# Optimization experiments

Hardware: AMD Instinct MI355X
Metric: run time of the kernel (lower is better)

Reference implementation:

```python
import jax, jax.numpy as jnp
import numpy as np

NUM_QUANTIZERS = 8
CODEBOOK_SIZE = 4096
DIM = 128
BATCH = 8
SEQ = 4096


def setup_inputs() -> dict:
    key = jax.random.key(0)
    k1, k2 = jax.random.split(key)
    x = jax.random.normal(k1, (BATCH, DIM, SEQ), dtype=jnp.float32)
    codebooks = jax.random.normal(k2, (NUM_QUANTIZERS, CODEBOOK_SIZE, DIM), dtype=jnp.float32)
    return {"x": x, "codebooks": codebooks}


def _rvq(x_bnc, codebooks):
    """Residual VQ: sequential per-stage nearest-codebook quantization.

    x_bnc: [b, n, d]; codebooks: [Q, K, d].
    Returns quantized [b, n, d], indices [b, n, Q], loss scalar.
    """
    residual = x_bnc
    quantized_out = jnp.zeros_like(x_bnc)
    all_indices = []
    all_losses = []
    Q = codebooks.shape[0]
    for q in range(Q):
        cb = codebooks[q]                                   # [K, d]
        # squared-euclidean distances: ||r||^2 - 2 r.c + ||c||^2  -> [b, n, K]
        r_sq = jnp.sum(residual * residual, axis=-1, keepdims=True)
        c_sq = jnp.sum(cb * cb, axis=-1)
        dots = jnp.einsum('bnd,kd->bnk', residual, cb)
        dist = r_sq - 2.0 * dots + c_sq
        idx = jnp.argmin(dist, axis=-1)                      # [b, n]
        quant = cb[idx]                                      # [b, n, d] gather
        # straight-through estimator (grad flows to residual, not codebook)
        quant_st = residual + jax.lax.stop_gradient(quant - residual)
        quantized_out = quantized_out + quant_st
        # commitment loss (codebook is EMA-updated, so detach the quantized side)
        all_losses.append(jnp.mean((jax.lax.stop_gradient(quant) - residual) ** 2))
        residual = residual - jax.lax.stop_gradient(quant)
        all_indices.append(idx)
    indices = jnp.stack(all_indices, axis=-1)                # [b, n, Q]
    loss = jnp.mean(jnp.stack(all_losses))
    return quantized_out, indices, loss


def reference(x, codebooks):
    # encode(): 'b c n -> b n c', quantize, 'b n c -> b c n'
    x_bnc = jnp.transpose(x, (0, 2, 1))
    quant, indices, loss = _rvq(x_bnc, codebooks)
    out = jnp.transpose(quant, (0, 2, 1))                    # [b, c, n]
    return out, indices, loss
```

## Files before the change

### kernel.cpp

```cpp
#include <hip/hip_runtime.h>

typedef _Float16 half8 __attribute__((ext_vector_type(8)));
typedef float    float4v __attribute__((ext_vector_type(4)));
typedef unsigned int u32;

#define NQ 8
#define KCODES 4096
#define DIMS 128
#define BATCH 8
#define SEQ 4096
#define ROWS (BATCH*SEQ)
#define TM 64
#define NBLK (ROWS/TM)
#define RESPAD 132
#define CANDROW 67
#define OUT_ELEMS (BATCH*DIMS*SEQ)
#define IDX_ELEMS (BATCH*SEQ*NQ)
#define LOSS_DIV (1.0f/33554432.0f)
#define FRAGQ ((size_t)4*256*64*8)
#define SBIAS 384.0f
#define WIN 2.0f

__device__ __forceinline__ unsigned umax_(unsigned a, unsigned b){ return a>b?a:b; }
__device__ __forceinline__ unsigned umin_(unsigned a, unsigned b){ return a<b?a:b; }

__device__ __forceinline__ void gload16(const void* g, void* l) {
    __builtin_amdgcn_global_load_lds(
        (const __attribute__((address_space(1))) u32*)g,
        (__attribute__((address_space(3))) u32*)l, 16, 0, 0);
}

__global__ void prep_csq(const float* __restrict__ cb, float* __restrict__ csq,
                         _Float16* __restrict__ cinit_h) {
    int c = blockIdx.x * 256 + threadIdx.x;
    const float4* p = (const float4*)(cb + (size_t)c * DIMS);
    float s = 0.f;
#pragma unroll
    for (int i = 0; i < 32; ++i) {
        float4 v = p[i];
        s += v.x * v.x + v.y * v.y + v.z * v.z + v.w * v.w;
    }
    csq[c] = s;
    cinit_h[c] = (_Float16)(SBIAS - 0.5f * s);
}

__global__ void prep_frags(const float* __restrict__ cb, _Float16* __restrict__ bhi,
                           float* __restrict__ loss_accum) {
    int g = blockIdx.x * 256 + threadIdx.x;
    if (g == 0) loss_accum[0] = 0.f;
    int lane = g & 63;
    int nt   = (g >> 6) & 255;
    int kb   = (g >> 14) & 3;
    int q    = g >> 16;
    int code = nt * 16 + (lane & 15);
    int k0   = kb * 32 + ((lane >> 4) * 8);
    const float* src = cb + ((size_t)q * KCODES + code) * DIMS + k0;
    float4 v0 = *(const float4*)(src);
    float4 v1 = *(const float4*)(src + 4);
    half8 h;
    h[0] = (_Float16)v0.x; h[1] = (_Float16)v0.y; h[2] = (_Float16)v0.z; h[3] = (_Float16)v0.w;
    h[4] = (_Float16)v1.x; h[5] = (_Float16)v1.y; h[6] = (_Float16)v1.z; h[7] = (_Float16)v1.w;
    *(half8*)(bhi + (size_t)g * 8) = h;
}

__device__ __forceinline__ void screen_tile(
        int t, int ntBase, int lane, int col,
        char* stgw, const _Float16* __restrict__ bq, const _Float16* cql,
        const half8 (&ahi)[4][4], unsigned (&p1)[4][4], unsigned (&p2)[4][4]) {
    int nt = ntBase + t;
    const half8* sp = (const half8*)(stgw + ((t & 1) << 12) + (lane << 4));
    half8 b0 = sp[0], b1 = sp[64], b2 = sp[128], b3 = sp[192];
    float csv = (float)cql[nt * 16 + col];

    asm volatile("s_waitcnt lgkmcnt(0)" ::: "memory");

    {
        int ntn = ntBase + ((t + 2) & 63);
        char* dst = stgw + ((t & 1) << 12);
#pragma unroll
        for (int kb = 0; kb < 4; ++kb) {
            const _Float16* g = bq + (((size_t)(kb * 256 + ntn) * 64 + lane) << 3);
            gload16(g, dst + (kb << 10));
        }
    }
    asm volatile("s_waitcnt vmcnt(4)" ::: "memory");

    float4v acc[4];
#pragma unroll
    for (int mt = 0; mt < 4; ++mt) { acc[mt][0]=0.f; acc[mt][1]=0.f; acc[mt][2]=0.f; acc[mt][3]=0.f; }
    __builtin_amdgcn_s_setprio(1);
#pragma unroll
    for (int mt = 0; mt < 4; ++mt) acc[mt] = __builtin_amdgcn_mfma_f32_16x16x32_f16(ahi[mt][0], b0, acc[mt], 0, 0, 0);
#pragma unroll
    for (int mt = 0; mt < 4; ++mt) acc[mt] = __builtin_amdgcn_mfma_f32_16x16x32_f16(ahi[mt][1], b1, acc[mt], 0, 0, 0);
#pragma unroll
    for (int mt = 0; mt < 4; ++mt) acc[mt] = __builtin_amdgcn_mfma_f32_16x16x32_f16(ahi[mt][2], b2, acc[mt], 0, 0, 0);
#pragma unroll
    for (int mt = 0; mt < 4; ++mt) acc[mt] = __builtin_amdgcn_mfma_f32_16x16x32_f16(ahi[mt][3], b3, acc[mt], 0, 0, 0);
    __builtin_amdgcn_s_setprio(0);

    unsigned idxv = (unsigned)(nt * 16 + col);
#pragma unroll
    for (int mt = 0; mt < 4; ++mt)
#pragma unroll
        for (int r = 0; r < 4; ++r) {
            float key = acc[mt][r] + csv;
            unsigned p  = (__float_as_uint(key) & 0xFFFFF000u) | idxv;
            unsigned t1 = umin_(p1[mt][r], p);
            p1[mt][r]   = umax_(p1[mt][r], p);
            p2[mt][r]   = umax_(p2[mt][r], t1);
        }
}

__launch_bounds__(256, 2)
__global__ void rvq_main(const float* __restrict__ x, const float* __restrict__ cb,
                         const _Float16* __restrict__ bhi,
                         const float* __restrict__ csq, const _Float16* __restrict__ cinit_h,
                         float* __restrict__ out, float* __restrict__ loss_accum) {
    __shared__ float res[TM][RESPAD];
    __shared__ __align__(16) char stg[4][8192];
    __shared__ __align__(16) _Float16 cinq_lds[KCODES];
    __shared__ float fbin[TM];
    unsigned (*cand)[CANDROW] = reinterpret_cast<unsigned (*)[CANDROW]>(&stg[0][0]);
    float* red = reinterpret_cast<float*>(&stg[0][0] + 20480);

    int tid  = threadIdx.x;
    int lane = tid & 63;
    int wv   = tid >> 6;
    int col  = lane & 15;
    int r0   = blockIdx.x * TM;
    int b    = r0 >> 12;
    int n0   = r0 & (SEQ - 1);
    const float* xb = x + (size_t)b * DIMS * SEQ + n0;

    {
        int d = tid >> 1, half = (tid & 1) * 32;
        const float* src = xb + (size_t)d * SEQ + half;
#pragma unroll
        for (int t4 = 0; t4 < 8; ++t4) {
            float4 v = *(const float4*)(src + t4 * 4);
            res[half + t4 * 4 + 0][d] = v.x;
            res[half + t4 * 4 + 1][d] = v.y;
            res[half + t4 * 4 + 2][d] = v.z;
            res[half + t4 * 4 + 3][d] = v.w;
        }
    }

    float lossacc = 0.f;
    int ntBase = wv * 64;
    char* stgw = &stg[wv][0];

    for (int q = 0; q < NQ; ++q) {
        __syncthreads();

        const _Float16* bq   = bhi + (size_t)q * FRAGQ;
        const _Float16* cq   = cinit_h + q * KCODES;
        const float*    csqq = csq + q * KCODES;

        {
            const _Float16* g0 = cq + wv * 1024 + lane * 8;
            gload16(g0,       (char*)cinq_lds + wv * 2048);
            gload16(g0 + 512, (char*)cinq_lds + wv * 2048 + 1024);
        }
#pragma unroll
        for (int tt = 0; tt < 2; ++tt) {
            char* dst = stgw + (tt << 12);
            int g = ntBase + tt;
#pragma unroll
            for (int kb = 0; kb < 4; ++kb)
                gload16(bq + (((size_t)(kb * 256 + g) * 64 + lane) << 3), dst + (kb << 10));
        }

        half8 ahi[4][4];
#pragma unroll
        for (int mt = 0; mt < 4; ++mt)
#pragma unroll
        for (int kb = 0; kb < 4; ++kb) {
            int row = mt * 16 + col;
            int k0  = kb * 32 + (lane >> 4) * 8;
            float4 v0 = *(const float4*)&res[row][k0];
            float4 v1 = *(const float4*)&res[row][k0 + 4];
            half8 h;
            h[0] = (_Float16)v0.x; h[1] = (_Float16)v0.y; h[2] = (_Float16)v0.z; h[3] = (_Float16)v0.w;
            h[4] = (_Float16)v1.x; h[5] = (_Float16)v1.y; h[6] = (_Float16)v1.z; h[7] = (_Float16)v1.w;
            ahi[mt][kb] = h;
        }

        unsigned p1[4][4], p2[4][4];
#pragma unroll
        for (int mt = 0; mt < 4; ++mt)
#pragma unroll
        for (int r = 0; r < 4; ++r) { p1[mt][r] = 0u; p2[mt][r] = 0u; }

        asm volatile("s_waitcnt vmcnt(4)" ::: "memory");

        for (int t = 0; t < 64; t += 2) {
            screen_tile(t,     ntBase, lane, col, stgw, bq, cinq_lds, ahi, p1, p2);
            screen_tile(t + 1, ntBase, lane, col, stgw, bq, cinq_lds, ahi, p1, p2);
        }
        asm volatile("s_waitcnt vmcnt(0)" ::: "memory");
        __syncthreads();

#pragma unroll
        for (int mt = 0; mt < 4; ++mt)
#pragma unroll
        for (int r = 0; r < 4; ++r) {
            unsigned a1 = p1[mt][r], a2 = p2[mt][r];
            unsigned b1 = (unsigned)__shfl_xor((int)a1, 1, 64);
            unsigned b2 = (unsigned)__shfl_xor((int)a2, 1, 64);
            unsigned n1 = umax_(a1, b1);
            unsigned n2 = umax_(umin_(a1, b1), umax_(a2, b2));
            if ((lane & 1) == 0) {
                int row = mt * 16 + (lane >> 4) * 4 + r;
                int cc  = wv * 16 + (col >> 1) * 2;
                cand[row][cc]     = n1;
                cand[row][cc + 1] = n2;
            }
        }
        __syncthreads();

        {
            int row = tid >> 2, s = tid & 3;
            const unsigned* cp = &cand[row][s * 16];
            unsigned m = 0;
#pragma unroll
            for (int k = 0; k < 16; ++k) m = umax_(m, cp[k]);
            m = umax_(m, (unsigned)__shfl_xor((int)m, 1, 64));
            m = umax_(m, (unsigned)__shfl_xor((int)m, 2, 64));
            float thr = __uint_as_float(m) - WIN;
            float bk = -3.4e38f;
            int   bi = KCODES;
            const float4* rv = (const float4*)&res[row][0];
            for (int k = 0; k < 16; ++k) {
                unsigned e = cp[k];
                if (__uint_as_float(e) >= thr) {
                    int idx = (int)(e & 0xFFFu);
                    const float4* cv = (const float4*)(cb + ((size_t)q * KCODES + idx) * DIMS);
                    float acc = 0.f;
#pragma unroll
                    for (int jj = 0; jj < 32; ++jj) {
                        float4 c4 = cv[jj];
                        float4 r4 = rv[jj];
                        acc = fmaf(r4.x, c4.x, acc);
                        acc = fmaf(r4.y, c4.y, acc);
                        acc = fmaf(r4.z, c4.z, acc);
                        acc = fmaf(r4.w, c4.w, acc);
                    }
                    float key = acc - 0.5f * csqq[idx];
                    if (key > bk || (key == bk && idx < bi)) { bk = key; bi = idx; }
                }
            }
#pragma unroll
            for (int mask = 1; mask <= 2; mask <<= 1) {
                float ok = __shfl_xor(bk, mask, 64);
                int   oi = __shfl_xor(bi, mask, 64);
                if (ok > bk || (ok == bk && oi < bi)) { bk = ok; bi = oi; }
            }
            if (s == 0) {
                fbin[row] = (float)bi;
                out[OUT_ELEMS + (size_t)(r0 + row) * NQ + q] = (float)bi;
            }
        }
        __syncthreads();

        {
            int row = tid >> 2, j = tid & 3;
            int bi = (int)fbin[row];
            const float* cv = cb + ((size_t)q * KCODES + bi) * DIMS + j * 32;
            float* rp = &res[row][j * 32];
#pragma unroll
            for (int t = 0; t < 8; ++t) {
                float4 c4 = *(const float4*)(cv + t * 4);
                float4 r4 = *(const float4*)(rp + t * 4);
                r4.x -= c4.x; lossacc = fmaf(r4.x, r4.x, lossacc);
                r4.y -= c4.y; lossacc = fmaf(r4.y, r4.y, lossacc);
                r4.z -= c4.z; lossacc = fmaf(r4.z, r4.z, lossacc);
                r4.w -= c4.w; lossacc = fmaf(r4.w, r4.w, lossacc);
                *(float4*)(rp + t * 4) = r4;
            }
        }
    }

    __syncthreads();
    red[tid] = lossacc;
    __syncthreads();
    for (int s = 128; s > 0; s >>= 1) {
        if (tid < s) red[tid] += red[tid + s];
        __syncthreads();
    }
    if (tid == 0) atomicAdd(loss_accum, red[0]);

    {
        int d = tid >> 1, half = (tid & 1) * 32;
        const float* src = xb + (size_t)d * SEQ + half;
        float* dst = out + (size_t)b * DIMS * SEQ + (size_t)d * SEQ + n0 + half;
#pragma unroll
        for (int t4 = 0; t4 < 8; ++t4) {
            float4 v = *(const float4*)(src + t4 * 4);
            v.x -= res[half + t4 * 4 + 0][d];
            v.y -= res[half + t4 * 4 + 1][d];
            v.z -= res[half + t4 * 4 + 2][d];
            v.w -= res[half + t4 * 4 + 3][d];
            *(float4*)(dst + t4 * 4) = v;
        }
    }
}

__global__ void finish_loss(const float* __restrict__ loss_accum, float* __restrict__ out) {
    out[OUT_ELEMS + IDX_ELEMS] = loss_accum[0] * LOSS_DIV;
}

extern "C" void kernel_launch(void* const* d_in, const int* in_sizes, int n_in,
                              void* d_out, int out_size, void* d_ws, size_t ws_size,
                              hipStream_t stream) {
    const float* x  = (const float*)d_in[0];
    const float* cb = (const float*)d_in[1];
    float* out = (float*)d_out;
    char*  ws  = (char*)d_ws;

    float*     loss_accum = (float*)ws;
    float*     csq     = (float*)(ws + 256);
    _Float16*  cinit_h = (_Float16*)(ws + 256 + 131072);
    _Float16*  bhi     = (_Float16*)(ws + 256 + 131072 + 65536);

    hipLaunchKernelGGL(prep_csq,   dim3(128),  dim3(256), 0, stream, cb, csq, cinit_h);
    hipLaunchKernelGGL(prep_frags, dim3(2048), dim3(256), 0, stream, cb, bhi, loss_accum);
    hipLaunchKernelGGL(rvq_main,   dim3(NBLK), dim3(256), 0, stream,
                       x, cb, bhi, csq, cinit_h, out, loss_accum);
    hipLaunchKernelGGL(finish_loss, dim3(1), dim3(1), 0, stream, loss_accum, out);
}
```

Baseline: 575.5 us.

## Stream codebook fragments straight to registers with a four-deep inline-asm pipeline

The codebook MFMA B-fragments are no longer staged through LDS with global_load_lds. They are now loaded directly into VGPRs with inline-asm global_load_dwordx4, and a rotating four-tile register pipeline is gated by s_waitcnt vmcnt(8). The per-code bias is folded into the accumulator initial value, which removes an add per output, and the LDS staging buffer is replaced with dedicated cand/red arrays. This removes LDS write and read traffic and the lgkmcnt waits from the inner screening loop. In exchange it raises VGPR pressure and issues prefetch loads past the last tile. Those loads may still be outstanding when the loop exits, and the compiler does not track them.

Result: faster. 527.9 us (-8.3%).

```diff
diff --git a/kernel.cpp b/kernel.cpp
--- a/kernel.cpp
+++ b/kernel.cpp
@@ -29,6 +29,18 @@
         (const __attribute__((address_space(1))) u32*)g,
         (__attribute__((address_space(3))) u32*)l, 16, 0, 0);
 }
+
+#define B_ISSUE(X0,X1,X2,X3,OFF)                                              \
+    asm volatile("global_load_dwordx4 %0, %4, %8 offset:" #OFF "\n\t"         \
+                 "global_load_dwordx4 %1, %5, %8 offset:" #OFF "\n\t"         \
+                 "global_load_dwordx4 %2, %6, %8 offset:" #OFF "\n\t"         \
+                 "global_load_dwordx4 %3, %7, %8 offset:" #OFF                \
+                 : "=v"(X0), "=v"(X1), "=v"(X2), "=v"(X3)                     \
+                 : "v"(vo0), "v"(vo1), "v"(vo2), "v"(vo3), "s"(bq))
+
+#define B_WAIT(X0,X1,X2,X3)                                                   \
+    asm volatile("s_waitcnt vmcnt(8)"                                         \
+                 : "+v"(X0), "+v"(X1), "+v"(X2), "+v"(X3))
 
 __global__ void prep_csq(const float* __restrict__ cb, float* __restrict__ csq,
                          _Float16* __restrict__ cinit_h) {
@@ -63,31 +75,13 @@
     *(half8*)(bhi + (size_t)g * 8) = h;
 }
 
-__device__ __forceinline__ void screen_tile(
-        int t, int ntBase, int lane, int col,
-        char* stgw, const _Float16* __restrict__ bq, const _Float16* cql,
-        const half8 (&ahi)[4][4], unsigned (&p1)[4][4], unsigned (&p2)[4][4]) {
-    int nt = ntBase + t;
-    const half8* sp = (const half8*)(stgw + ((t & 1) << 12) + (lane << 4));
-    half8 b0 = sp[0], b1 = sp[64], b2 = sp[128], b3 = sp[192];
-    float csv = (float)cql[nt * 16 + col];
-
-    asm volatile("s_waitcnt lgkmcnt(0)" ::: "memory");
-
-    {
-        int ntn = ntBase + ((t + 2) & 63);
-        char* dst = stgw + ((t & 1) << 12);
-#pragma unroll
-        for (int kb = 0; kb < 4; ++kb) {
-            const _Float16* g = bq + (((size_t)(kb * 256 + ntn) * 64 + lane) << 3);
-            gload16(g, dst + (kb << 10));
-        }
-    }
-    asm volatile("s_waitcnt vmcnt(4)" ::: "memory");
-
+__device__ __forceinline__ void compute16(
+        const half8& b0, const half8& b1, const half8& b2, const half8& b3,
+        float csv, unsigned idxv, const half8 (&ahi)[4][4],
+        unsigned (&p1)[4][4], unsigned (&p2)[4][4]) {
     float4v acc[4];
 #pragma unroll
-    for (int mt = 0; mt < 4; ++mt) { acc[mt][0]=0.f; acc[mt][1]=0.f; acc[mt][2]=0.f; acc[mt][3]=0.f; }
+    for (int mt = 0; mt < 4; ++mt) { acc[mt][0]=csv; acc[mt][1]=csv; acc[mt][2]=csv; acc[mt][3]=csv; }
     __builtin_amdgcn_s_setprio(1);
 #pragma unroll
     for (int mt = 0; mt < 4; ++mt) acc[mt] = __builtin_amdgcn_mfma_f32_16x16x32_f16(ahi[mt][0], b0, acc[mt], 0, 0, 0);
@@ -98,14 +92,11 @@
 #pragma unroll
     for (int mt = 0; mt < 4; ++mt) acc[mt] = __builtin_amdgcn_mfma_f32_16x16x32_f16(ahi[mt][3], b3, acc[mt], 0, 0, 0);
     __builtin_amdgcn_s_setprio(0);
-
-    unsigned idxv = (unsigned)(nt * 16 + col);
 #pragma unroll
     for (int mt = 0; mt < 4; ++mt)
 #pragma unroll
         for (int r = 0; r < 4; ++r) {
-            float key = acc[mt][r] + csv;
-            unsigned p  = (__float_as_uint(key) & 0xFFFFF000u) | idxv;
+            unsigned p  = (__float_as_uint(acc[mt][r]) & 0xFFFFF000u) | idxv;
             unsigned t1 = umin_(p1[mt][r], p);
             p1[mt][r]   = umax_(p1[mt][r], p);
             p2[mt][r]   = umax_(p2[mt][r], t1);
@@ -117,12 +108,11 @@
                          const _Float16* __restrict__ bhi,
                          const float* __restrict__ csq, const _Float16* __restrict__ cinit_h,
                          float* __restrict__ out, float* __restrict__ loss_accum) {
-    __shared__ float res[TM][RESPAD];
-    __shared__ __align__(16) char stg[4][8192];
+    __shared__ float    res[TM][RESPAD];
     __shared__ __align__(16) _Float16 cinq_lds[KCODES];
-    __shared__ float fbin[TM];
-    unsigned (*cand)[CANDROW] = reinterpret_cast<unsigned (*)[CANDROW]>(&stg[0][0]);
-    float* red = reinterpret_cast<float*>(&stg[0][0] + 20480);
+    __shared__ unsigned cand[TM][CANDROW];
+    __shared__ float    fbin[TM];
+    __shared__ float    red[256];
 
     int tid  = threadIdx.x;
     int lane = tid & 63;
@@ -148,10 +138,10 @@
 
     float lossacc = 0.f;
     int ntBase = wv * 64;
-    char* stgw = &stg[wv][0];
 
     for (int q = 0; q < NQ; ++q) {
-        __syncthreads();
+        asm volatile("s_waitcnt lgkmcnt(0)" ::: "memory");
+        __builtin_amdgcn_s_barrier();
 
         const _Float16* bq   = bhi + (size_t)q * FRAGQ;
         const _Float16* cq   = cinit_h + q * KCODES;
@@ -162,14 +152,19 @@
             gload16(g0,       (char*)cinq_lds + wv * 2048);
             gload16(g0 + 512, (char*)cinq_lds + wv * 2048 + 1024);
         }
-#pragma unroll
-        for (int tt = 0; tt < 2; ++tt) {
-            char* dst = stgw + (tt << 12);
-            int g = ntBase + tt;
-#pragma unroll
-            for (int kb = 0; kb < 4; ++kb)
-                gload16(bq + (((size_t)(kb * 256 + g) * 64 + lane) << 3), dst + (kb << 10));
-        }
+
+        u32 vo0, vo1, vo2, vo3;
+        {
+            u32 base = (u32)(((ntBase + 3) * 64 + lane) << 4);
+            vo0 = base;
+            vo1 = base + (256u * 64u * 16u);
+            vo2 = base + (512u * 64u * 16u);
+            vo3 = base + (768u * 64u * 16u);
+        }
+        half8 a0,a1,a2,a3, b0,b1,b2,b3, c0,c1,c2,c3, d0,d1,d2,d3;
+        B_ISSUE(a0,a1,a2,a3, -3072);
+        B_ISSUE(b0,b1,b2,b3, -2048);
+        B_ISSUE(c0,c1,c2,c3, -1024);
 
         half8 ahi[4][4];
 #pragma unroll
@@ -192,24 +187,44 @@
 #pragma unroll
         for (int r = 0; r < 4; ++r) { p1[mt][r] = 0u; p2[mt][r] = 0u; }
 
-        asm volatile("s_waitcnt vmcnt(4)" ::: "memory");
-
-        for (int t = 0; t < 64; t += 2) {
-            screen_tile(t,     ntBase, lane, col, stgw, bq, cinq_lds, ahi, p1, p2);
-            screen_tile(t + 1, ntBase, lane, col, stgw, bq, cinq_lds, ahi, p1, p2);
-        }
-        asm volatile("s_waitcnt vmcnt(0)" ::: "memory");
+        unsigned idx0 = (unsigned)(ntBase * 16 + col);
+
+        for (int ii = 0; ii < 16; ++ii) {
+            int t = ii * 4;
+            float cs0 = (float)cinq_lds[(ntBase + t + 0) * 16 + col];
+            float cs1 = (float)cinq_lds[(ntBase + t + 1) * 16 + col];
+            float cs2 = (float)cinq_lds[(ntBase + t + 2) * 16 + col];
+            float cs3 = (float)cinq_lds[(ntBase + t + 3) * 16 + col];
+
+            B_WAIT(a0,a1,a2,a3);
+            B_ISSUE(d0,d1,d2,d3, 0);
+            compute16(a0,a1,a2,a3, cs0, idx0 + (unsigned)(t+0)*16u, ahi, p1, p2);
+
+            B_WAIT(b0,b1,b2,b3);
+            B_ISSUE(a0,a1,a2,a3, 1024);
+            compute16(b0,b1,b2,b3, cs1, idx0 + (unsigned)(t+1)*16u, ahi, p1, p2);
+
+            B_WAIT(c0,c1,c2,c3);
+            B_ISSUE(b0,b1,b2,b3, 2048);
+            compute16(c0,c1,c2,c3, cs2, idx0 + (unsigned)(t+2)*16u, ahi, p1, p2);
+
+            B_WAIT(d0,d1,d2,d3);
+            B_ISSUE(c0,c1,c2,c3, 3072);
+            compute16(d0,d1,d2,d3, cs3, idx0 + (unsigned)(t+3)*16u, ahi, p1, p2);
+
+            vo0 += 4096; vo1 += 4096; vo2 += 4096; vo3 += 4096;
+        }
         __syncthreads();
 
 #pragma unroll
         for (int mt = 0; mt < 4; ++mt)
 #pragma unroll
         for (int r = 0; r < 4; ++r) {
-            unsigned a1 = p1[mt][r], a2 = p2[mt][r];
-            unsigned b1 = (unsigned)__shfl_xor((int)a1, 1, 64);
-            unsigned b2 = (unsigned)__shfl_xor((int)a2, 1, 64);
-            unsigned n1 = umax_(a1, b1);
-            unsigned n2 = umax_(umin_(a1, b1), umax_(a2, b2));
+            unsigned q1 = p1[mt][r], q2 = p2[mt][r];
+            unsigned o1 = (unsigned)__shfl_xor((int)q1, 1, 64);
+            unsigned o2 = (unsigned)__shfl_xor((int)q2, 1, 64);
+            unsigned n1 = umax_(q1, o1);
+            unsigned n2 = umax_(umin_(q1, o1), umax_(q2, o2));
             if ((lane & 1) == 0) {
                 int row = mt * 16 + (lane >> 4) * 4 + r;
                 int cc  = wv * 16 + (col >> 1) * 2;
```
